# Optimization experiments

Hardware: AMD Instinct MI355X
Metric: run time of the kernel (lower is better)

The kernel has to match this reference:

```python
import jax, jax.numpy as jnp
import numpy as np

D = 2        # dof (input_dim of fc1)
H1 = 64      # hidden width
N = 262144   # batch
NEG_SLOPE = -0.01  # NOTE: original uses self.neg_slope=-0.01 in the analytic derivative
                   # while the forward activation uses F.leaky_relu default slope +0.01.
                   # We replicate this exactly.

def _lin_init(k, out_d, in_d):
    bound = 1.0 / np.sqrt(in_d)
    kw, kb = jax.random.split(k)
    W = jax.random.uniform(kw, (out_d, in_d), minval=-bound, maxval=bound, dtype=jnp.float32)
    b = jax.random.uniform(kb, (out_d,), minval=-bound, maxval=bound, dtype=jnp.float32)
    return W, b

def setup_inputs():
    key = jax.random.key(0)
    ks = jax.random.split(key, 6)
    W1, b1 = _lin_init(ks[0], H1, D)
    W1a, b1a = _lin_init(ks[1], H1, H1)
    W2, b2 = _lin_init(ks[2], D, H1)
    W3, b3 = _lin_init(ks[3], D, H1)
    W4, b4 = _lin_init(ks[4], 1, H1)
    x = jax.random.normal(ks[5], (N, 3 * D), dtype=jnp.float32)
    return {"x": x, "W1": W1, "b1": b1, "W1a": W1a, "b1a": b1a,
            "W2": W2, "b2": b2, "W3": W3, "b3": b3, "W4": W4, "b4": b4}

def _forward(x, W1, b1, W1a, b1a, W2, b2, W3, b3, W4, b4):
    n = x.shape[0]
    d = x.shape[1] // 3
    q, qd, qdd = x[:, :d], x[:, d:2 * d], x[:, 2 * d:]

    h1 = jax.nn.leaky_relu(q @ W1.T + b1, 0.01)       # [n,H1]
    h2 = jax.nn.leaky_relu(h1 @ W1a.T + b1a, 0.01)    # [n,H1]
    g = h2 @ W2.T + b2                                # [n,d]
    ld = jax.nn.relu(h2 @ W3.T + b3)                  # [n,d]  diagonal of L
    lo = h2 @ W4.T + b4                               # [n,1]  off-diagonal(s)

    # Analytic Jacobians. diag_embed(a) @ W == a[:,:,None] * W (no [n,H,H] materialization).
    dR1 = jnp.where(h1 > 0, 1.0, NEG_SLOPE)
    dh1_dq = dR1[:, :, None] * W1[None]                              # [n,H1,d]
    dR2 = jnp.where(h2 > 0, 1.0, NEG_SLOPE)
    dh2_dq = dR2[:, :, None] * jnp.einsum('hk,nkd->nhd', W1a, dh1_dq)  # [n,H1,d]
    dR3 = jnp.where(ld > 0, 1.0, 0.0)
    dld_dq = dR3[:, :, None] * jnp.einsum('oh,nhd->nod', W3, dh2_dq)   # [n,d,d]
    dlo_dq = jnp.einsum('oh,nhd->nod', W4, dh2_dq)                     # [n,1,d]

    dld_dqi = jnp.transpose(dld_dq, (0, 2, 1))[..., None]  # [n,d,d,1]
    dlo_dqi = jnp.transpose(dlo_dq, (0, 2, 1))[..., None]  # [n,d,1,1]
    dld_dt = dld_dq @ qd[:, :, None]                       # [n,d,1]
    dlo_dt = dlo_dq @ qd[:, :, None]                       # [n,1,1]

    zeros = jnp.zeros_like(ld)
    zeros2 = jnp.zeros_like(dld_dqi)
    Lc, dLt, dLq = [], [], []
    s, e = 0, d - 1
    for i in range(d):  # loop over d (=2) columns of the Cholesky factor
        Lc.append(jnp.concatenate([zeros[:, :i], ld[:, i:i + 1], lo[:, s:e]], axis=1))
        dLt.append(jnp.concatenate([zeros[:, :i], dld_dt[:, i].reshape(n, 1),
                                    dlo_dt[:, s:e].reshape(n, -1)], axis=1))
        dLq.append(jnp.concatenate([zeros2[:, :, :i].reshape(n, d, -1),
                                    dld_dqi[:, :, i].reshape(n, d, 1),
                                    dlo_dqi[:, :, s:e].reshape(n, d, -1)], axis=2))
        s, e = s + e, e + d - 2 - i
    L = jnp.stack(Lc, axis=2)                                    # [n,d,d]
    dL_dt = jnp.stack(dLt, axis=2)                               # [n,d,d]
    dL_dqi = jnp.transpose(jnp.stack(dLq, axis=3), (0, 2, 3, 1)) # [n,d,d,d]

    eps = 1e-5
    Lt = jnp.swapaxes(L, 1, 2)
    Hm = L @ Lt + eps * jnp.eye(d, dtype=x.dtype)
    dH_dt = L @ jnp.swapaxes(dL_dt, 1, 2) + dL_dt @ Lt

    qts = []
    for i in range(d):
        A = dL_dqi[..., i] @ Lt + L @ jnp.swapaxes(dL_dqi[..., i], 1, 2)
        qts.append(qd[:, None, :] @ A @ qd[:, :, None])  # [n,1,1]
    quad = jnp.stack(qts, axis=1).reshape(n, d, 1)

    c = dH_dt @ qd[:, :, None] - 0.5 * quad
    tau = Hm @ qdd[:, :, None] + c + g[:, :, None]
    return tau[..., 0], Hm, c[..., 0], g

def reference(x, W1, b1, W1a, b1a, W2, b2, W3, b3, W4, b4):
    return _forward(x, W1, b1, W1a, b1a, W2, b2, W3, b3, W4, b4)
```

## Files before the change

kernel.cpp:

```cpp
#include <hip/hip_runtime.h>
#include <stdint.h>


typedef __attribute__((ext_vector_type(8))) _Float16 f16x8;
typedef __attribute__((ext_vector_type(4))) float f32x4;

#define MFMA16(A, B, C) __builtin_amdgcn_mfma_f32_16x16x32_f16((A), (B), (C), 0, 0, 0)

__global__ __launch_bounds__(256, 3) void delan_fwd(
    const float* __restrict__ x,
    const float* __restrict__ W1,  const float* __restrict__ b1,
    const float* __restrict__ W1a, const float* __restrict__ b1a,
    const float* __restrict__ W2,  const float* __restrict__ b2,
    const float* __restrict__ W3,  const float* __restrict__ b3,
    const float* __restrict__ W4,  const float* __restrict__ b4,
    float* __restrict__ out, int n_total)
{
    __shared__ _Float16 afrag[2][4][2][64][8];
    __shared__ float w1b1[64][4];
    __shared__ float cst[6][64];

    const int tid  = threadIdx.x;
    const int lane = tid & 63;
    const int wid  = tid >> 6;
    const int p    = lane & 15;
    const int qrt  = lane >> 4;
    const int n    = blockIdx.x * 256 + tid;
    const int nc   = (n < n_total) ? n : (n_total - 1);

    const float2 xa = *(const float2*)(x + 6 * nc);
    const float2 xb = *(const float2*)(x + 6 * nc + 2);
    const float2 xc = *(const float2*)(x + 6 * nc + 4);
    const float x0 = xa.x, x1 = xa.y;
    const float x2 = xb.x, x3 = xb.y;
    const float x4 = xc.x, x5 = xc.y;

    if (tid < 64) {
        const int k = tid;
        w1b1[k][0] = W1[2*k]; w1b1[k][1] = W1[2*k+1]; w1b1[k][2] = b1[k]; w1b1[k][3] = 0.f;
        cst[0][k] = W2[k];      cst[1][k] = W2[64 + k];
        cst[2][k] = W3[k];      cst[3][k] = W3[64 + k];
        cst[4][k] = W4[k];      cst[5][k] = b1a[k];
    }
    {
        const int ht = wid;
#pragma unroll
        for (int kh = 0; kh < 2; ++kh) {
            const int row = ht * 16 + p;
            const int kb  = kh * 32 + qrt * 8;
            float wv[8];
            *(float4*)&wv[0] = *(const float4*)(W1a + row * 64 + kb);
            *(float4*)&wv[4] = *(const float4*)(W1a + row * 64 + kb + 4);
            f16x8 hi, lo;
#pragma unroll
            for (int j = 0; j < 8; ++j) {
                const _Float16 h = (_Float16)wv[j];
                hi[j] = h;
                lo[j] = (_Float16)((wv[j] - (float)h) * 4096.0f);
            }
            *(f16x8*)&afrag[0][ht][kh][lane][0] = hi;
            *(f16x8*)&afrag[1][ht][kh][lane][0] = lo;
        }
    }
    __syncthreads();

    float fg0=0.f, fg1=0.f, fl0=0.f, fl1=0.f, foo=0.f;
    float fp00=0.f, fp01=0.f, fp10=0.f, fp11=0.f, fr0=0.f, fr1=0.f;

#pragma unroll
    for (int t = 0; t < 4; ++t) {
        const float q0t = __shfl(x0, t * 16 + p);
        const float q1t = __shfl(x1, t * 16 + p);
        f16x8 Bhh[2], Bhl[2], Bu0[2], Bu1[2];
#pragma unroll
        for (int kh = 0; kh < 2; ++kh) {
#pragma unroll
            for (int j = 0; j < 8; ++j) {
                const int k = kh * 32 + qrt * 8 + j;
                const f32x4 wv = *(const f32x4*)&w1b1[k][0];
                const float pre = fmaf(wv[0], q0t, fmaf(wv[1], q1t, wv[2]));
                const bool pos = pre > 0.0f;
                const float h1v = pos ? pre : 0.01f * pre;
                const float u0v = pos ? wv[0] : -0.01f * wv[0];
                const float u1v = pos ? wv[1] : -0.01f * wv[1];
                const _Float16 hh = (_Float16)h1v;
                Bhh[kh][j] = hh;
                Bhl[kh][j] = (_Float16)((h1v - (float)hh) * 4096.0f);
                Bu0[kh][j] = (_Float16)u0v;
                Bu1[kh][j] = (_Float16)u1v;
            }
        }

        float ag0=0.f, ag1=0.f, al0=0.f, al1=0.f, aoo=0.f;
        float ap00=0.f, ap01=0.f, ap10=0.f, ap11=0.f, ar0=0.f, ar1=0.f;
#pragma unroll
        for (int ht = 0; ht < 4; ++ht) {
            const f16x8 Ah0 = *(const f16x8*)&afrag[0][ht][0][lane][0];
            const f16x8 Ah1 = *(const f16x8*)&afrag[0][ht][1][lane][0];
            const f16x8 Al0 = *(const f16x8*)&afrag[1][ht][0][lane][0];
            const f16x8 Al1 = *(const f16x8*)&afrag[1][ht][1][lane][0];
            f32x4 Chi = {0.f,0.f,0.f,0.f}, Clo = {0.f,0.f,0.f,0.f};
            f32x4 Cz0 = {0.f,0.f,0.f,0.f}, Cz1 = {0.f,0.f,0.f,0.f};
            Chi = MFMA16(Ah0, Bhh[0], Chi);  Chi = MFMA16(Ah1, Bhh[1], Chi);
            Clo = MFMA16(Ah0, Bhl[0], Clo);  Clo = MFMA16(Ah1, Bhl[1], Clo);
            Clo = MFMA16(Al0, Bhh[0], Clo);  Clo = MFMA16(Al1, Bhh[1], Clo);
            Cz0 = MFMA16(Ah0, Bu0[0], Cz0);  Cz0 = MFMA16(Ah1, Bu0[1], Cz0);
            Cz1 = MFMA16(Ah0, Bu1[0], Cz1);  Cz1 = MFMA16(Ah1, Bu1[1], Cz1);

            const int hb = ht * 16 + qrt * 4;
            const f32x4 w2a  = *(const f32x4*)&cst[0][hb];
            const f32x4 w2b  = *(const f32x4*)&cst[1][hb];
            const f32x4 w3a  = *(const f32x4*)&cst[2][hb];
            const f32x4 w3b  = *(const f32x4*)&cst[3][hb];
            const f32x4 w4v  = *(const f32x4*)&cst[4][hb];
            const f32x4 b1av = *(const f32x4*)&cst[5][hb];
#pragma unroll
            for (int r = 0; r < 4; ++r) {
                const float ah = fmaf(2.44140625e-4f, Clo[r], Chi[r]) + b1av[r];
                const bool pos = ah > 0.0f;
                const float h2 = pos ? ah : 0.01f * ah;
                ag0 = fmaf(w2a[r], h2, ag0);   ag1 = fmaf(w2b[r], h2, ag1);
                al0 = fmaf(w3a[r], h2, al0);   al1 = fmaf(w3b[r], h2, al1);
                aoo = fmaf(w4v[r], h2, aoo);
                const float z0 = Cz0[r], z1 = Cz1[r];
                const float d0 = pos ? z0 : -0.01f * z0;
                const float d1 = pos ? z1 : -0.01f * z1;
                ap00 = fmaf(w3a[r], d0, ap00); ap01 = fmaf(w3a[r], d1, ap01);
                ap10 = fmaf(w3b[r], d0, ap10); ap11 = fmaf(w3b[r], d1, ap11);
                ar0  = fmaf(w4v[r], d0, ar0);  ar1  = fmaf(w4v[r], d1, ar1);
            }
        }

#define RED(v) { v += __shfl_xor(v, 16); v += __shfl_xor(v, 32); }
        RED(ag0) RED(ag1) RED(al0) RED(al1) RED(aoo)
        RED(ap00) RED(ap01) RED(ap10) RED(ap11) RED(ar0) RED(ar1)
#undef RED
        if (qrt == t) {
            fg0 = ag0; fg1 = ag1; fl0 = al0; fl1 = al1; foo = aoo;
            fp00 = ap00; fp01 = ap01; fp10 = ap10; fp11 = ap11;
            fr0 = ar0; fr1 = ar1;
        }
    }

    const float g0 = fg0 + b2[0], g1 = fg1 + b2[1];
    const float l0 = fl0 + b3[0], l1 = fl1 + b3[1];
    const float oo = foo + b4[0];
    const float p00 = fp00, p01 = fp01, p10 = fp10, p11 = fp11;
    const float r0 = fr0, r1 = fr1;

    const float ld0 = fmaxf(l0, 0.0f);
    const float ld1 = fmaxf(l1, 0.0f);
    const float dr30 = (l0 > 0.0f) ? 1.0f : 0.0f;
    const float dr31 = (l1 > 0.0f) ? 1.0f : 0.0f;

    const float da00 = dr30 * p00, da01 = dr30 * p01;
    const float da10 = dr31 * p10, da11 = dr31 * p11;

    const float l00 = ld0, l10 = oo, l11 = ld1;

    const float m00 = da00 * x2 + da01 * x3;
    const float m11 = da10 * x2 + da11 * x3;
    const float m10 = r0  * x2 + r1  * x3;

    const float eps = 1e-5f;
    const float Hm00 = fmaf(l00, l00, eps);
    const float Hm01 = l00 * l10;
    const float Hm11 = fmaf(l10, l10, fmaf(l11, l11, eps));

    const float dH00 = 2.0f * l00 * m00;
    const float dH01 = fmaf(l00, m10, l10 * m00);
    const float dH11 = 2.0f * fmaf(l10, m10, l11 * m11);

    const float x22 = x2 * x2, x23 = x2 * x3, x33 = x3 * x3;
    const float quad0 = 2.0f * (da00 * l00 * x22
                      + (fmaf(da00, l10, r0 * l00)) * x23
                      + (fmaf(r0, l10, da10 * l11)) * x33);
    const float quad1 = 2.0f * (da01 * l00 * x22
                      + (fmaf(da01, l10, r1 * l00)) * x23
                      + (fmaf(r1, l10, da11 * l11)) * x33);

    const float c0 = fmaf(dH00, x2, dH01 * x3) - 0.5f * quad0;
    const float c1 = fmaf(dH01, x2, dH11 * x3) - 0.5f * quad1;

    const float tau0 = fmaf(Hm00, x4, Hm01 * x5) + c0 + g0;
    const float tau1 = fmaf(Hm01, x4, Hm11 * x5) + c1 + g1;

    if (n < n_total) {
        const long long N = n_total;
        float2* tau_out = (float2*)(out) + n;
        float4* hm_out  = (float4*)(out + 2 * N) + n;
        float2* c_out   = (float2*)(out + 6 * N) + n;
        float2* g_out   = (float2*)(out + 8 * N) + n;
        *tau_out = make_float2(tau0, tau1);
        *hm_out  = make_float4(Hm00, Hm01, Hm01, Hm11);
        *c_out   = make_float2(c0, c1);
        *g_out   = make_float2(g0, g1);
    }
}

extern "C" void kernel_launch(void* const* d_in, const int* in_sizes, int n_in,
                              void* d_out, int out_size, void* d_ws, size_t ws_size,
                              hipStream_t stream) {
    const float* x   = (const float*)d_in[0];
    const float* W1  = (const float*)d_in[1];
    const float* b1  = (const float*)d_in[2];
    const float* W1a = (const float*)d_in[3];
    const float* b1a = (const float*)d_in[4];
    const float* W2  = (const float*)d_in[5];
    const float* b2  = (const float*)d_in[6];
    const float* W3  = (const float*)d_in[7];
    const float* b3  = (const float*)d_in[8];
    const float* W4  = (const float*)d_in[9];
    const float* b4  = (const float*)d_in[10];
    float* out = (float*)d_out;

    const int n_total = in_sizes[0] / 6;
    const int block = 256;
    const int grid = (n_total + block - 1) / block;
    delan_fwd<<<grid, block, 0, stream>>>(x, W1, b1, W1a, b1a, W2, b2,
                                          W3, b3, W4, b4, out, n_total);
}
```

Baseline: 31.12 us.

## Pack layer-1 activation math into paired f32/f16 ops and permlane reductions

Rewrites the per-element layer-1 leaky-ReLU and fp16 hi/lo split using packed v_pk_fma/v_pk_mul f32 and v_pk_mul_f16 with a select-built slope mask. It also folds b1a into the MFMA accumulator init, replaces the shfl_xor quad reductions with permlane16/32 swaps, and raises the occupancy hint from 3 to 4 blocks per CU. The aim is to cut VALU instruction count and cross-lane shuffle latency. It risks slight precision differences from round-toward-zero pkrtz conversions, and register pressure under the tighter launch bound.

```diff
diff --git a/kernel.cpp b/kernel.cpp
--- a/kernel.cpp
+++ b/kernel.cpp
@@ -4,10 +4,36 @@
 
 typedef __attribute__((ext_vector_type(8))) _Float16 f16x8;
 typedef __attribute__((ext_vector_type(4))) float f32x4;
-
-#define MFMA16(A, B, C) __builtin_amdgcn_mfma_f32_16x16x32_f16((A), (B), (C), 0, 0, 0)
-
-__global__ __launch_bounds__(256, 3) void delan_fwd(
+typedef __attribute__((ext_vector_type(2))) float f32x2;
+typedef __attribute__((ext_vector_type(4))) unsigned int u32x4;
+
+#define MFMA16(A,B,C) __builtin_amdgcn_mfma_f32_16x16x32_f16((A),(B),(C),0,0,0)
+
+static __device__ __forceinline__ f32x2 pk_fma(f32x2 a, f32x2 b, f32x2 c) {
+    f32x2 d;
+    asm("v_pk_fma_f32 %0, %1, %2, %3" : "=v"(d) : "v"(a), "v"(b), "v"(c));
+    return d;
+}
+static __device__ __forceinline__ f32x2 pk_mul(f32x2 a, f32x2 b) {
+    f32x2 d;
+    asm("v_pk_mul_f32 %0, %1, %2" : "=v"(d) : "v"(a), "v"(b));
+    return d;
+}
+static __device__ __forceinline__ unsigned pkmul16(unsigned a, unsigned b) {
+    unsigned d;
+    asm("v_pk_mul_f16 %0, %1, %2" : "=v"(d) : "v"(a), "v"(b));
+    return d;
+}
+static __device__ __forceinline__ float qsum(float v) {
+    float a = v, b = v;
+    asm("v_permlane16_swap_b32 %0, %1" : "+v"(a), "+v"(b));
+    const float s = a + b;
+    float c = s, d = s;
+    asm("v_permlane32_swap_b32 %0, %1" : "+v"(c), "+v"(d));
+    return c + d;
+}
+
+__global__ __launch_bounds__(256, 4) void delan_fwd(
     const float* __restrict__ x,
     const float* __restrict__ W1,  const float* __restrict__ b1,
     const float* __restrict__ W1a, const float* __restrict__ b1a,
@@ -17,7 +43,7 @@
     float* __restrict__ out, int n_total)
 {
     __shared__ _Float16 afrag[2][4][2][64][8];
-    __shared__ float w1b1[64][4];
+    __shared__ float w0s[64], w1s[64], bs[64];
     __shared__ float cst[6][64];
 
     const int tid  = threadIdx.x;
@@ -37,7 +63,7 @@
 
     if (tid < 64) {
         const int k = tid;
-        w1b1[k][0] = W1[2*k]; w1b1[k][1] = W1[2*k+1]; w1b1[k][2] = b1[k]; w1b1[k][3] = 0.f;
+        w0s[k] = W1[2*k]; w1s[k] = W1[2*k+1]; bs[k] = b1[k];
         cst[0][k] = W2[k];      cst[1][k] = W2[64 + k];
         cst[2][k] = W3[k];      cst[3][k] = W3[64 + k];
         cst[4][k] = W4[k];      cst[5][k] = b1a[k];
@@ -64,6 +90,9 @@
     }
     __syncthreads();
 
+    const f32x2 c4096  = {4096.0f, 4096.0f};
+    const f32x2 cm4096 = {-4096.0f, -4096.0f};
+
     float fg0=0.f, fg1=0.f, fl0=0.f, fl1=0.f, foo=0.f;
     float fp00=0.f, fp01=0.f, fp10=0.f, fp11=0.f, fr0=0.f, fr1=0.f;
 
@@ -71,23 +100,42 @@
     for (int t = 0; t < 4; ++t) {
         const float q0t = __shfl(x0, t * 16 + p);
         const float q1t = __shfl(x1, t * 16 + p);
-        f16x8 Bhh[2], Bhl[2], Bu0[2], Bu1[2];
+        const f32x2 q00 = {q0t, q0t};
+        const f32x2 q11 = {q1t, q1t};
+        u32x4 Bhh[2], Bhl[2], Bu0[2], Bu1[2];
 #pragma unroll
         for (int kh = 0; kh < 2; ++kh) {
-#pragma unroll
-            for (int j = 0; j < 8; ++j) {
-                const int k = kh * 32 + qrt * 8 + j;
-                const f32x4 wv = *(const f32x4*)&w1b1[k][0];
-                const float pre = fmaf(wv[0], q0t, fmaf(wv[1], q1t, wv[2]));
-                const bool pos = pre > 0.0f;
-                const float h1v = pos ? pre : 0.01f * pre;
-                const float u0v = pos ? wv[0] : -0.01f * wv[0];
-                const float u1v = pos ? wv[1] : -0.01f * wv[1];
-                const _Float16 hh = (_Float16)h1v;
-                Bhh[kh][j] = hh;
-                Bhl[kh][j] = (_Float16)((h1v - (float)hh) * 4096.0f);
-                Bu0[kh][j] = (_Float16)u0v;
-                Bu1[kh][j] = (_Float16)u1v;
+            const int kb = kh * 32 + qrt * 8;
+#pragma unroll
+            for (int c = 0; c < 4; ++c) {
+                const f32x2 w0p = *(const f32x2*)&w0s[kb + 2*c];
+                const f32x2 w1p = *(const f32x2*)&w1s[kb + 2*c];
+                const f32x2 bp  = *(const f32x2*)&bs [kb + 2*c];
+                const f32x2 prep = pk_fma(w0p, q00, pk_fma(w1p, q11, bp));
+                const bool pos0 = prep.x > 0.0f;
+                const bool pos1 = prep.y > 0.0f;
+                const unsigned mlo = pos0 ? 0x00003C00u : 0x0000A11Fu;
+                const unsigned mhi = pos1 ? 0x3C000000u : 0xA11F0000u;
+                const unsigned drw = mlo | mhi;
+                const unsigned p0w = __builtin_bit_cast(unsigned,
+                    __builtin_amdgcn_cvt_pkrtz(w0p.x, w0p.y));
+                const unsigned p1w = __builtin_bit_cast(unsigned,
+                    __builtin_amdgcn_cvt_pkrtz(w1p.x, w1p.y));
+                Bu0[kh][c] = pkmul16(p0w, drw);
+                Bu1[kh][c] = pkmul16(p1w, drw);
+                f32x2 sp;
+                sp.x = pos0 ? 1.0f : 0.01f;
+                sp.y = pos1 ? 1.0f : 0.01f;
+                const f32x2 h1p = pk_mul(prep, sp);
+                const auto hhv = __builtin_amdgcn_cvt_pkrtz(h1p.x, h1p.y);
+                Bhh[kh][c] = __builtin_bit_cast(unsigned, hhv);
+                f32x2 hf;
+                hf.x = (float)hhv[0];
+                hf.y = (float)hhv[1];
+                const f32x2 tt = pk_mul(h1p, c4096);
+                const f32x2 rp = pk_fma(hf, cm4096, tt);
+                Bhl[kh][c] = __builtin_bit_cast(unsigned,
+                    __builtin_amdgcn_cvt_pkrtz(rp.x, rp.y));
             }
         }
 
@@ -99,24 +147,34 @@
             const f16x8 Ah1 = *(const f16x8*)&afrag[0][ht][1][lane][0];
             const f16x8 Al0 = *(const f16x8*)&afrag[1][ht][0][lane][0];
             const f16x8 Al1 = *(const f16x8*)&afrag[1][ht][1][lane][0];
-            f32x4 Chi = {0.f,0.f,0.f,0.f}, Clo = {0.f,0.f,0.f,0.f};
-            f32x4 Cz0 = {0.f,0.f,0.f,0.f}, Cz1 = {0.f,0.f,0.f,0.f};
-            Chi = MFMA16(Ah0, Bhh[0], Chi);  Chi = MFMA16(Ah1, Bhh[1], Chi);
-            Clo = MFMA16(Ah0, Bhl[0], Clo);  Clo = MFMA16(Ah1, Bhl[1], Clo);
-            Clo = MFMA16(Al0, Bhh[0], Clo);  Clo = MFMA16(Al1, Bhh[1], Clo);
-            Cz0 = MFMA16(Ah0, Bu0[0], Cz0);  Cz0 = MFMA16(Ah1, Bu0[1], Cz0);
-            Cz1 = MFMA16(Ah0, Bu1[0], Cz1);  Cz1 = MFMA16(Ah1, Bu1[1], Cz1);
+            const f16x8 bh0 = __builtin_bit_cast(f16x8, Bhh[0]);
+            const f16x8 bh1 = __builtin_bit_cast(f16x8, Bhh[1]);
+            const f16x8 bl0 = __builtin_bit_cast(f16x8, Bhl[0]);
+            const f16x8 bl1 = __builtin_bit_cast(f16x8, Bhl[1]);
+            const f16x8 bu00 = __builtin_bit_cast(f16x8, Bu0[0]);
+            const f16x8 bu01 = __builtin_bit_cast(f16x8, Bu0[1]);
+            const f16x8 bu10 = __builtin_bit_cast(f16x8, Bu1[0]);
+            const f16x8 bu11 = __builtin_bit_cast(f16x8, Bu1[1]);
 
             const int hb = ht * 16 + qrt * 4;
+            f32x4 Chi = *(const f32x4*)&cst[5][hb];
+            f32x4 Clo = {0.f,0.f,0.f,0.f};
+            f32x4 Cz0 = {0.f,0.f,0.f,0.f};
+            f32x4 Cz1 = {0.f,0.f,0.f,0.f};
+            Chi = MFMA16(Ah0, bh0, Chi);  Chi = MFMA16(Ah1, bh1, Chi);
+            Clo = MFMA16(Ah0, bl0, Clo);  Clo = MFMA16(Ah1, bl1, Clo);
+            Clo = MFMA16(Al0, bh0, Clo);  Clo = MFMA16(Al1, bh1, Clo);
+            Cz0 = MFMA16(Ah0, bu00, Cz0); Cz0 = MFMA16(Ah1, bu01, Cz0);
+            Cz1 = MFMA16(Ah0, bu10, Cz1); Cz1 = MFMA16(Ah1, bu11, Cz1);
+
             const f32x4 w2a  = *(const f32x4*)&cst[0][hb];
             const f32x4 w2b  = *(const f32x4*)&cst[1][hb];
             const f32x4 w3a  = *(const f32x4*)&cst[2][hb];
             const f32x4 w3b  = *(const f32x4*)&cst[3][hb];
             const f32x4 w4v  = *(const f32x4*)&cst[4][hb];
-            const f32x4 b1av = *(const f32x4*)&cst[5][hb];
 #pragma unroll
             for (int r = 0; r < 4; ++r) {
-                const float ah = fmaf(2.44140625e-4f, Clo[r], Chi[r]) + b1av[r];
+                const float ah = fmaf(2.44140625e-4f, Clo[r], Chi[r]);
                 const bool pos = ah > 0.0f;
                 const float h2 = pos ? ah : 0.01f * ah;
                 ag0 = fmaf(w2a[r], h2, ag0);   ag1 = fmaf(w2b[r], h2, ag1);
@@ -131,10 +189,10 @@
             }
         }
 
-#define RED(v) { v += __shfl_xor(v, 16); v += __shfl_xor(v, 32); }
-        RED(ag0) RED(ag1) RED(al0) RED(al1) RED(aoo)
-        RED(ap00) RED(ap01) RED(ap10) RED(ap11) RED(ar0) RED(ar1)
-#undef RED
+        ag0 = qsum(ag0); ag1 = qsum(ag1); al0 = qsum(al0); al1 = qsum(al1);
+        aoo = qsum(aoo);
+        ap00 = qsum(ap00); ap01 = qsum(ap01); ap10 = qsum(ap10); ap11 = qsum(ap11);
+        ar0 = qsum(ar0);  ar1 = qsum(ar1);
         if (qrt == t) {
             fg0 = ag0; fg1 = ag1; fl0 = al0; fl1 = al1; foo = aoo;
             fp00 = ap00; fp01 = ap01; fp10 = ap10; fp11 = ap11;
```

Result: faster. 30.31 us (-2.6%).
